# Kernel tuning notes

Hardware: AMD Instinct MI355X
Metric: run time of the kernel (lower is better)

The kernel has to match this reference:

```python
import jax, jax.numpy as jnp
import numpy as np

B, S, D, H, F = 64, 256, 512, 8, 2048
NB = 2
L = NB + 2 * NB  # blocks_1 (NB) + blocks_2 (2*NB) = 6 attention layers
DH = D // H
FC1, FC2 = 512, 256  # final_fc_dim, final_fc_dim // 2


def setup_inputs() -> dict:
    key = jax.random.key(0)
    ks = jax.random.split(key, 32)
    w = lambda k, shape, s: jax.random.normal(k, shape, dtype=jnp.float32) * s
    sD = D ** -0.5
    return {
        "q_embed_data": w(ks[0], (B, S, D), 1.0),
        "qa_embed_data": w(ks[1], (B, S, D), 1.0),
        "Wq": w(ks[2], (L, D, D), sD), "bq": jnp.zeros((L, D), jnp.float32),
        "Wk": w(ks[3], (L, D, D), sD), "bk": jnp.zeros((L, D), jnp.float32),
        "Wv": w(ks[4], (L, D, D), sD), "bv": jnp.zeros((L, D), jnp.float32),
        "Wo": w(ks[5], (L, D, D), sD), "bo": jnp.zeros((L, D), jnp.float32),
        "gammas": w(ks[6], (L, H), 1.0),
        "ln1_g": jnp.ones((L, D), jnp.float32), "ln1_b": jnp.zeros((L, D), jnp.float32),
        "W1": w(ks[7], (L, D, F), sD), "b1": jnp.zeros((L, F), jnp.float32),
        "W2": w(ks[8], (L, F, D), F ** -0.5), "b2": jnp.zeros((L, D), jnp.float32),
        "ln2_g": jnp.ones((L, D), jnp.float32), "ln2_b": jnp.zeros((L, D), jnp.float32),
        "O1": w(ks[9], (2 * D, FC1), (2 * D) ** -0.5), "bO1": jnp.zeros((FC1,), jnp.float32),
        "O2": w(ks[10], (FC1, FC2), FC1 ** -0.5), "bO2": jnp.zeros((FC2,), jnp.float32),
        "O3": w(ks[11], (FC2, 1), FC2 ** -0.5), "bO3": jnp.zeros((1,), jnp.float32),
    }


def _layer_norm(x, g, b):
    mu = x.mean(-1, keepdims=True)
    var = ((x - mu) ** 2).mean(-1, keepdims=True)
    return (x - mu) * jax.lax.rsqrt(var + 1e-5) * g + b


def _akt_attention(q, k, v, mask, gamma, zero_pad):
    # q,k,v: [B,H,S,DH]; mask: [S,S] bool; gamma: [H]
    neg = jnp.float32(-1e32)
    scores = jnp.einsum('bhqd,bhkd->bhqk', q, k) / np.sqrt(DH).astype(np.float32)
    # monotonic distance-decay (detached in the original): softmax'd scores -> cumulative distance
    sm = jax.nn.softmax(jnp.where(mask, scores, neg), axis=-1) * mask
    sm = jax.lax.stop_gradient(sm)
    distcum = jnp.cumsum(sm, axis=-1)
    disttot = jnp.sum(sm, axis=-1, keepdims=True)
    idx = jnp.arange(S)
    pos = jnp.abs(idx[:, None] - idx[None, :]).astype(jnp.float32)  # |x1 - x2|
    dist = jnp.sqrt(jnp.clip((disttot - distcum) * pos, 0.0, None))
    g = -jax.nn.softplus(gamma)[None, :, None, None]
    total_effect = jnp.clip(jnp.exp(dist * g), 1e-5, 1e5)
    scores = jnp.where(mask, scores * total_effect, neg)
    attn = jax.nn.softmax(scores, axis=-1)
    if zero_pad:
        attn = attn.at[:, :, 0, :].set(0.0)  # zero first query row
    out = jnp.einsum('bhqk,bhkd->bhqd', attn, v)
    return out, attn


def reference(q_embed_data, qa_embed_data, Wq, bq, Wk, bk, Wv, bv, Wo, bo, gammas,
              ln1_g, ln1_b, W1, b1, W2, b2, ln2_g, ln2_b, O1, bO1, O2, bO2, O3, bO3):
    idx = jnp.arange(S)
    mask_incl = idx[:, None] >= idx[None, :]  # mask==1: current + past
    mask_excl = idx[:, None] > idx[None, :]   # mask==0: strictly past

    def block(i, query, key_, vals, incl, zero_pad, apply_pos):
        proj = lambda x, W, b: (x @ W + b).reshape(B, S, H, DH).transpose(0, 2, 1, 3)
        qh, kh, vh = proj(query, Wq[i], bq[i]), proj(key_, Wk[i], bk[i]), proj(vals, Wv[i], bv[i])
        o, attn = _akt_attention(qh, kh, vh, mask_incl if incl else mask_excl, gammas[i], zero_pad)
        o = o.transpose(0, 2, 1, 3).reshape(B, S, D) @ Wo[i] + bo[i]
        q2 = _layer_norm(query + o, ln1_g[i], ln1_b[i])
        if apply_pos:
            h = jax.nn.relu(q2 @ W1[i] + b1[i]) @ W2[i] + b2[i]
            q2 = _layer_norm(q2 + h, ln2_g[i], ln2_b[i])
        return q2, attn

    y = qa_embed_data
    x = q_embed_data
    li = 0
    for _ in range(NB):  # blocks_1: knowledge encoder, self-attn, mask=1
        y, _ = block(li, y, y, y, incl=True, zero_pad=False, apply_pos=True)
        li += 1
    attn = None
    flag_first = True
    for _ in range(2 * NB):  # blocks_2: alternating question self-attn / knowledge retriever
        if flag_first:
            x, _ = block(li, x, x, x, incl=True, zero_pad=False, apply_pos=False)
            flag_first = False
        else:
            x, attn = block(li, x, x, y, incl=False, zero_pad=True, apply_pos=True)
            flag_first = True
        li += 1

    concat_q = jnp.concatenate([x, q_embed_data], axis=-1)  # [B,S,2D]
    h = jax.nn.relu(concat_q @ O1 + bO1)
    h = jax.nn.relu(h @ O2 + bO2)
    preds = jax.nn.sigmoid((h @ O3 + bO3)[..., 0])  # [B,S]
    return preds
```

## Files before the change

kernel.cpp:

```cpp
#include <hip/hip_runtime.h>

typedef unsigned short u16;
typedef unsigned int u32;
typedef short short8 __attribute__((ext_vector_type(8)));
typedef float f32x4 __attribute__((ext_vector_type(4)));

#define DEV static __device__ __forceinline__

DEV u16 f2bf(float f) {
  u32 u = __builtin_bit_cast(u32, f);
  u32 r = u + 0x7FFFu + ((u >> 16) & 1u);
  return (u16)(r >> 16);
}
DEV float bf2f(u16 h) { u32 u = ((u32)h) << 16; return __builtin_bit_cast(float, u); }

DEV u32 cvtpk(float lo, float hi_) {
  u32 r;
  asm("v_cvt_pk_bf16_f32 %0, %1, %2" : "=v"(r) : "v"(lo), "v"(hi_));
  return r;
}

DEV void async16(const u16* g, u16* l) {
  __builtin_amdgcn_global_load_lds((const __attribute__((address_space(1))) void*)g,
                                   (__attribute__((address_space(3))) void*)l, 16, 0, 0);
}

template<bool RELU, bool OUTBF, bool RESID, bool SPLIT3>
__global__ __launch_bounds__(256, 2) void gemm_kernel(
    const u16* __restrict__ A, const u16* __restrict__ A2, int KA,
    int lda, int lda2,
    const u16* __restrict__ Bt, int K,
    const float* __restrict__ bias, const float* __restrict__ resid,
    float* __restrict__ Cf, u16* __restrict__ Cb, u16* __restrict__ Cb2, u16* __restrict__ Cb3,
    int ldc)
{
  __shared__ u16 smem[2][16384];
  const int tid = threadIdx.x, wave = tid >> 6, lane = tid & 63;
  const int m0 = blockIdx.x * 128, n0 = blockIdx.y * 128;
  const int wr = wave >> 1, wc = wave & 1;
  const int lj = lane & 15, hi = lane >> 4;

  f32x4 acc[4][4];
  const f32x4 zz = {0.f, 0.f, 0.f, 0.f};
#pragma unroll
  for (int i = 0; i < 4; i++)
#pragma unroll
    for (int j = 0; j < 4; j++) acc[i][j] = zz;

  const int nkt = K / 64;

  auto stage = [&](int buf, int kt) {
    int kofs = kt * 64;
    const u16* sa; int la;
    if (kofs < KA) { sa = A + kofs; la = lda; }
    else           { sa = A2 + (kofs - KA); la = lda2; }
#pragma unroll
    for (int i = 0; i < 8; i++) {
      int c = wave * 8 + i;
      if (c < 16) {
        const u16* g = sa + (size_t)(m0 + c * 8 + (lane >> 3)) * la + (lane & 7) * 8;
        async16(g, &smem[buf][c * 512]);
      } else {
        const u16* g = Bt + (size_t)(n0 + (c - 16) * 8 + (lane >> 3)) * K + kofs + (lane & 7) * 8;
        async16(g, &smem[buf][c * 512]);
      }
    }
  };

  stage(0, 0);
  int cur = 0;
  for (int kt = 0; kt < nkt; kt++) {
    __syncthreads();
    if (kt + 1 < nkt) stage(cur ^ 1, kt + 1);
    const u16* la_ = &smem[cur][0];
    const u16* lb_ = &smem[cur][8192];
#pragma unroll
    for (int ks = 0; ks < 2; ks++) {
      short8 af[4], bfr[4];
#pragma unroll
      for (int mi = 0; mi < 4; mi++)
        af[mi] = *(const short8*)(la_ + (wr * 64 + mi * 16 + lj) * 64 + ks * 32 + hi * 8);
#pragma unroll
      for (int ni = 0; ni < 4; ni++)
        bfr[ni] = *(const short8*)(lb_ + (wc * 64 + ni * 16 + lj) * 64 + ks * 32 + hi * 8);
#pragma unroll
      for (int mi = 0; mi < 4; mi++)
#pragma unroll
        for (int ni = 0; ni < 4; ni++)
          acc[mi][ni] = __builtin_amdgcn_mfma_f32_16x16x32_bf16(af[mi], bfr[ni], acc[mi][ni], 0, 0, 0);
    }
    cur ^= 1;
  }

  u16* outB = Cb;
  int nloc = n0;
  if (SPLIT3) {
    int sec = n0 >> 9;
    outB = (sec == 0) ? Cb : (sec == 1) ? Cb2 : Cb3;
    nloc = n0 & 511;
  }

  float bv[4];
#pragma unroll
  for (int ni = 0; ni < 4; ni++) bv[ni] = bias[n0 + wc * 64 + ni * 16 + lj];
#pragma unroll
  for (int mi = 0; mi < 4; mi++)
#pragma unroll
    for (int r = 0; r < 4; r++) {
      int row = m0 + wr * 64 + mi * 16 + hi * 4 + r;
      size_t rb = (size_t)row * ldc;
#pragma unroll
      for (int ni = 0; ni < 4; ni++) {
        int col = nloc + wc * 64 + ni * 16 + lj;
        float v = acc[mi][ni][r] + bv[ni];
        if (RESID) v += resid[rb + col];
        if (RELU) v = fmaxf(v, 0.f);
        if (OUTBF) outB[rb + col] = f2bf(v);
        else Cf[rb + col] = v;
      }
    }
}

template<bool INCL, bool ZP>
__global__ __launch_bounds__(512) void attn_kernel(
    const u16* __restrict__ qb, const u16* __restrict__ kb, const u16* __restrict__ vb,
    u16* __restrict__ ob, const float* __restrict__ gammas, int li)
{
  __shared__ u16 smem[32768];
  const int tid = threadIdx.x, wave = tid >> 6, lane = tid & 63;
  const int h = blockIdx.x, b = blockIdx.y;
  const int lj = lane & 15, hi = lane >> 4;
  const size_t rowbase = (size_t)b * 256 * 512 + h * 64;

#pragma unroll
  for (int p = 0; p < 2; p++) {
    int r2 = p * 128 + (tid >> 3) * 2;
    int cc = (tid & 7) * 8;
    union { uint4 v; u16 e[8]; } v0, v1;
    uint4 k0 = *(const uint4*)(kb + rowbase + (size_t)r2 * 512 + cc);
    uint4 k1 = *(const uint4*)(kb + rowbase + (size_t)(r2 + 1) * 512 + cc);
    v0.v = *(const uint4*)(vb + rowbase + (size_t)r2 * 512 + cc);
    v1.v = *(const uint4*)(vb + rowbase + (size_t)(r2 + 1) * 512 + cc);
    *(uint4*)((char*)smem + r2 * 128 + ((cc * 2) ^ ((r2 & 7) << 4))) = k0;
    *(uint4*)((char*)smem + (r2 + 1) * 128 + ((cc * 2) ^ (((r2 + 1) & 7) << 4))) = k1;
#pragma unroll
    for (int i = 0; i < 8; i++) {
      int d = cc + i;
      u32 pk = (u32)v0.e[i] | ((u32)v1.e[i] << 16);
      *(u32*)((char*)smem + 32768 + d * 512 + ((2 * r2) ^ ((d & 7) << 4))) = pk;
    }
  }

  const int qt0 = wave, qt1 = 15 - wave;

  short8 qfa[2][2];
#pragma unroll
  for (int cf = 0; cf < 2; cf++) {
    int t = cf ? qt1 : qt0;
#pragma unroll
    for (int s = 0; s < 2; s++)
      qfa[cf][s] = *(const short8*)(qb + rowbase + (size_t)(t * 16 + lj) * 512 + s * 32 + hi * 8);
  }

  float gm = gammas[li * 8 + h];
  float geff = -(gm > 20.f ? gm : log1pf(__expf(gm)));

  __syncthreads();

  const f32x4 zz = {0.f, 0.f, 0.f, 0.f};
  const int hsel = hi >> 1;
  const int sbase = lj + 32 * (hi & 1);

#pragma unroll
  for (int cf = 0; cf < 2; cf++) {
    const int t = cf ? qt1 : qt0;
    const int qb0 = t * 16;
    const int q = qb0 + lj;
    const int nrf = t + 1;
    const int nsp = (t + 2) >> 1;

    f32x4 acc[16], E[16];
#pragma unroll
    for (int rf = 0; rf < 16; rf++) acc[rf] = zz;

#pragma unroll
    for (int rf = 0; rf < 16; rf++) {
      if (rf >= nrf) continue;
      int row = rf * 16 + lj;
#pragma unroll
      for (int s = 0; s < 2; s++) {
        short8 kf = *(const short8*)((char*)smem + row * 128 + ((s * 64 + hi * 16) ^ ((row & 7) << 4)));
        acc[rf] = __builtin_amdgcn_mfma_f32_16x16x32_bf16(kf, qfa[cf][s], acc[rf], 0, 0, 0);
      }
    }

    float mx = -1e30f;
#pragma unroll
    for (int rf = 0; rf < 16; rf++) {
      if (rf >= nrf) continue;
#pragma unroll
      for (int r = 0; r < 4; r++) {
        acc[rf][r] *= 0.125f;
        int k = rf * 16 + hi * 4 + r;
        bool valid = INCL ? (k <= q) : (k < q);
        mx = fmaxf(mx, valid ? acc[rf][r] : -1e30f);
      }
    }
    mx = fmaxf(mx, __shfl_xor(mx, 16));
    mx = fmaxf(mx, __shfl_xor(mx, 32));
    float sum = 0.f;
#pragma unroll
    for (int rf = 0; rf < 16; rf++) {
      if (rf >= nrf) continue;
#pragma unroll
      for (int r = 0; r < 4; r++) {
        int k = rf * 16 + hi * 4 + r;
        bool valid = INCL ? (k <= q) : (k < q);
        float ev = valid ? __expf(acc[rf][r] - mx) : 0.f;
        E[rf][r] = ev;
        sum += ev;
      }
    }
    sum += __shfl_xor(sum, 16);
    sum += __shfl_xor(sum, 32);
    float inv1 = sum > 0.f ? 1.f / sum : 0.f;
    float dtot = sum > 0.f ? 1.f : 0.f;

    float run = 0.f;
#pragma unroll
    for (int rf = 0; rf < 16; rf++) {
      if (rf >= nrf) continue;
      float p[4];
      float pa = 0.f;
#pragma unroll
      for (int r = 0; r < 4; r++) {
        pa += E[rf][r] * inv1;
        p[r] = pa;
      }
      float tl = p[3];
      float v = tl;
      float u1 = __shfl_up(v, 16); v += (hi >= 1) ? u1 : 0.f;
      float u2 = __shfl_up(v, 32); v += (hi >= 2) ? u2 : 0.f;
      float T = __shfl(v, lj + 48);
      float cbase = run + (v - tl);
#pragma unroll
      for (int r = 0; r < 4; r++) {
        int k = rf * 16 + hi * 4 + r;
        bool valid = INCL ? (k <= q) : (k < q);
        float tail = fmaxf(dtot - (cbase + p[r]), 0.f);
        float pos = (float)(q - k);
        float dist = sqrtf(tail * pos);
        float te = fmaxf(__expf(dist * geff), 1e-5f);
        acc[rf][r] = valid ? acc[rf][r] * te : -1e32f;
      }
      run += T;
    }

    float mx2 = -3.0e38f;
#pragma unroll
    for (int rf = 0; rf < 16; rf++) {
      if (rf >= nrf) continue;
#pragma unroll
      for (int r = 0; r < 4; r++) mx2 = fmaxf(mx2, acc[rf][r]);
    }
    mx2 = fmaxf(mx2, __shfl_xor(mx2, 16));
    mx2 = fmaxf(mx2, __shfl_xor(mx2, 32));
    float sum2 = 0.f;
#pragma unroll
    for (int rf = 0; rf < 16; rf++) {
      if (rf >= nrf) continue;
#pragma unroll
      for (int r = 0; r < 4; r++) {
        float ev = __expf(acc[rf][r] - mx2);
        acc[rf][r] = ev;
        sum2 += ev;
      }
    }
    sum2 += __shfl_xor(sum2, 16);
    sum2 += __shfl_xor(sum2, 32);
    float inv = 1.f / sum2;
    if (ZP) { if (q == 0) inv = 0.f; }
#pragma unroll
    for (int rf = 0; rf < 16; rf++) {
      if (rf >= nrf) continue;
#pragma unroll
      for (int r = 0; r < 4; r++) acc[rf][r] *= inv;
    }

    f32x4 oacc[4];
#pragma unroll
    for (int j = 0; j < 4; j++) oacc[j] = zz;

#pragma unroll
    for (int sp = 0; sp < 8; sp++) {
      if (sp >= nsp) continue;
      u32 a0 = cvtpk(acc[2 * sp][0],     acc[2 * sp][1]);
      u32 a1 = cvtpk(acc[2 * sp][2],     acc[2 * sp][3]);
      u32 b0 = cvtpk(acc[2 * sp + 1][0], acc[2 * sp + 1][1]);
      u32 b1 = cvtpk(acc[2 * sp + 1][2], acc[2 * sp + 1][3]);
      u32 pw[4];
#pragma unroll
      for (int tt = 0; tt < 4; tt++) {
        int src = sbase + 16 * (tt >> 1);
        u32 za = (u32)__shfl((int)((tt & 1) ? a1 : a0), src);
        u32 zb = (u32)__shfl((int)((tt & 1) ? b1 : b0), src);
        pw[tt] = hsel ? zb : za;
      }
      short8 pf = __builtin_bit_cast(short8, *(uint4*)pw);
#pragma unroll
      for (int nf = 0; nf < 4; nf++) {
        int d = nf * 16 + lj;
        short8 vf = *(const short8*)((char*)smem + 32768 + d * 512 + ((sp * 64 + hi * 16) ^ ((d & 7) << 4)));
        oacc[nf] = __builtin_amdgcn_mfma_f32_16x16x32_bf16(pf, vf, oacc[nf], 0, 0, 0);
      }
    }

#pragma unroll
    for (int r = 0; r < 4; r++) {
      int qr = qb0 + hi * 4 + r;
      size_t obase = (size_t)(b * 256 + qr) * 512 + h * 64;
#pragma unroll
      for (int nf = 0; nf < 4; nf++)
        ob[obase + nf * 16 + lj] = f2bf(oacc[nf][r]);
    }
  }
}

__global__ __launch_bounds__(256) void ln_kernel(const float* __restrict__ x,
    const float* __restrict__ g, const float* __restrict__ bt,
    float* __restrict__ outF, u16* __restrict__ outB)
{
  int row = blockIdx.x * 4 + (threadIdx.x >> 6), lane = threadIdx.x & 63;
  const float* xr = x + (size_t)row * 512 + lane * 8;
  float4 a = *(const float4*)xr;
  float4 c = *(const float4*)(xr + 4);
  float s = a.x + a.y + a.z + a.w + c.x + c.y + c.z + c.w;
  float q = a.x*a.x + a.y*a.y + a.z*a.z + a.w*a.w + c.x*c.x + c.y*c.y + c.z*c.z + c.w*c.w;
#pragma unroll
  for (int m = 1; m <= 32; m <<= 1) { s += __shfl_xor(s, m); q += __shfl_xor(q, m); }
  float mu = s * (1.f / 512.f);
  float var = q * (1.f / 512.f) - mu * mu;
  float rs = rsqrtf(fmaxf(var, 0.f) + 1e-5f);
  const float* gr = g + lane * 8; const float* br = bt + lane * 8;
  float4 g0 = *(const float4*)gr, g1v = *(const float4*)(gr + 4);
  float4 b0 = *(const float4*)br, b1v = *(const float4*)(br + 4);
  float y[8];
  y[0]=(a.x-mu)*rs*g0.x+b0.x; y[1]=(a.y-mu)*rs*g0.y+b0.y; y[2]=(a.z-mu)*rs*g0.z+b0.z; y[3]=(a.w-mu)*rs*g0.w+b0.w;
  y[4]=(c.x-mu)*rs*g1v.x+b1v.x; y[5]=(c.y-mu)*rs*g1v.y+b1v.y; y[6]=(c.z-mu)*rs*g1v.z+b1v.z; y[7]=(c.w-mu)*rs*g1v.w+b1v.w;
  float* of = outF + (size_t)row * 512 + lane * 8;
  *(float4*)of = make_float4(y[0], y[1], y[2], y[3]);
  *(float4*)(of + 4) = make_float4(y[4], y[5], y[6], y[7]);
  union { uint4 v; u16 e[8]; } pk;
#pragma unroll
  for (int i = 0; i < 8; i++) pk.e[i] = f2bf(y[i]);
  *(uint4*)(outB + (size_t)row * 512 + lane * 8) = pk.v;
}

__global__ void cvt_kernel(const float* __restrict__ in, u16* __restrict__ out, int n8)
{
  int i = blockIdx.x * 256 + threadIdx.x;
  if (i >= n8) return;
  float4 a = ((const float4*)in)[2 * i], c = ((const float4*)in)[2 * i + 1];
  union { uint4 v; u16 e[8]; } pk;
  pk.e[0]=f2bf(a.x); pk.e[1]=f2bf(a.y); pk.e[2]=f2bf(a.z); pk.e[3]=f2bf(a.w);
  pk.e[4]=f2bf(c.x); pk.e[5]=f2bf(c.y); pk.e[6]=f2bf(c.z); pk.e[7]=f2bf(c.w);
  ((uint4*)out)[i] = pk.v;
}

__global__ void trans_kernel(const float* __restrict__ in, u16* __restrict__ out,
                             int R, int C, size_t istr, size_t ostr)
{
  __shared__ float tile[32][33];
  in += (size_t)blockIdx.z * istr;
  out += (size_t)blockIdx.z * ostr;
  int c0 = blockIdx.x * 32, r0 = blockIdx.y * 32;
  int tx = threadIdx.x & 31, ty = threadIdx.x >> 5;
#pragma unroll
  for (int i = 0; i < 4; i++) tile[ty + i * 8][tx] = in[(size_t)(r0 + ty + i * 8) * C + c0 + tx];
  __syncthreads();
#pragma unroll
  for (int i = 0; i < 4; i++) out[(size_t)(c0 + ty + i * 8) * R + r0 + tx] = f2bf(tile[tx][ty + i * 8]);
}

__global__ void bias_concat_kernel(const float* __restrict__ bq, const float* __restrict__ bk,
                                   const float* __restrict__ bv, float* __restrict__ out)
{
  int t = blockIdx.x * 256 + threadIdx.x;
  if (t >= 6 * 1536) return;
  int li = t / 1536, c = t % 1536;
  float v = (c < 512) ? bq[li * 512 + c]
          : (c < 1024) ? bk[li * 512 + c - 512]
                       : bv[li * 512 + c - 1024];
  out[t] = v;
}

__global__ __launch_bounds__(256) void pred_kernel(const u16* __restrict__ h2,
    const float* __restrict__ O3, const float* __restrict__ bO3, float* __restrict__ out)
{
  int row = blockIdx.x * 4 + (threadIdx.x >> 6), lane = threadIdx.x & 63;
  union { uint2 v; u16 e[4]; } hv;
  hv.v = *(const uint2*)(h2 + (size_t)row * 256 + lane * 4);
  float d = 0.f;
#pragma unroll
  for (int i = 0; i < 4; i++) d += bf2f(hv.e[i]) * O3[lane * 4 + i];
#pragma unroll
  for (int m = 1; m <= 32; m <<= 1) d += __shfl_xor(d, m);
  if (lane == 0) out[row] = 1.f / (1.f + expf(-(d + bO3[0])));
}

extern "C" void kernel_launch(void* const* d_in, const int* in_sizes, int n_in,
                              void* d_out, int out_size, void* d_ws, size_t ws_size,
                              hipStream_t stream)
{
  const float* qe   = (const float*)d_in[0];
  const float* qa   = (const float*)d_in[1];
  const float* Wq   = (const float*)d_in[2];  const float* bq  = (const float*)d_in[3];
  const float* Wk   = (const float*)d_in[4];  const float* bk  = (const float*)d_in[5];
  const float* Wv   = (const float*)d_in[6];  const float* bv  = (const float*)d_in[7];
  const float* Wo   = (const float*)d_in[8];  const float* bo  = (const float*)d_in[9];
  const float* gam  = (const float*)d_in[10];
  const float* ln1g = (const float*)d_in[11]; const float* ln1b = (const float*)d_in[12];
  const float* W1   = (const float*)d_in[13]; const float* b1  = (const float*)d_in[14];
  const float* W2   = (const float*)d_in[15]; const float* b2  = (const float*)d_in[16];
  const float* ln2g = (const float*)d_in[17]; const float* ln2b = (const float*)d_in[18];
  const float* O1   = (const float*)d_in[19]; const float* bO1 = (const float*)d_in[20];
  const float* O2   = (const float*)d_in[21]; const float* bO2 = (const float*)d_in[22];
  const float* O3   = (const float*)d_in[23]; const float* bO3 = (const float*)d_in[24];
  float* preds = (float*)d_out;

  const int M = 16384;
  const int BIG = 0x3fffffff;
  char* ws = (char*)d_ws;
  size_t off = 0;
  auto alloc = [&](size_t bytes) { char* p = ws + off; off += (bytes + 255) & ~(size_t)255; return p; };

  u16* wqkvt = (u16*)alloc((size_t)6*1536*512*2);
  u16* wot   = (u16*)alloc((size_t)6*512*512*2);
  u16* w1t   = (u16*)alloc((size_t)6*2048*512*2);
  u16* w2t   = (u16*)alloc((size_t)6*512*2048*2);
  u16* o1t   = (u16*)alloc((size_t)512*1024*2);
  u16* o2t   = (u16*)alloc((size_t)256*512*2);
  float* bqkv = (float*)alloc((size_t)6*1536*4);
  u16* qx  = (u16*)alloc((size_t)M*512*2);
  u16* sA  = (u16*)alloc((size_t)M*512*2);
  u16* sB  = (u16*)alloc((size_t)M*512*2);
  float* g1 = (float*)alloc((size_t)M*512*4);
  u16* region = (u16*)alloc((size_t)M*2048*2);
  u16* qbf = region;
  u16* kbf = region + (size_t)M*512;
  u16* vbf = region + (size_t)2*M*512;
  u16* obf = region + (size_t)3*M*512;
  u16* h1  = region;
  u16* hd1 = region;
  u16* hd2 = region + (size_t)2*M*512;
  (void)ws_size; (void)in_sizes; (void)n_in; (void)out_size;

  trans_kernel<<<dim3(16, 16, 6), 256, 0, stream>>>(Wq, wqkvt,                          512, 512,  (size_t)512*512,  (size_t)1536*512);
  trans_kernel<<<dim3(16, 16, 6), 256, 0, stream>>>(Wk, wqkvt + (size_t)512*512,        512, 512,  (size_t)512*512,  (size_t)1536*512);
  trans_kernel<<<dim3(16, 16, 6), 256, 0, stream>>>(Wv, wqkvt + (size_t)1024*512,       512, 512,  (size_t)512*512,  (size_t)1536*512);
  trans_kernel<<<dim3(16, 16, 6), 256, 0, stream>>>(Wo, wot,                            512, 512,  (size_t)512*512,  (size_t)512*512);
  trans_kernel<<<dim3(64, 16, 6), 256, 0, stream>>>(W1, w1t,                            512, 2048, (size_t)512*2048, (size_t)2048*512);
  trans_kernel<<<dim3(16, 64, 6), 256, 0, stream>>>(W2, w2t,                            2048, 512, (size_t)2048*512, (size_t)512*2048);
  trans_kernel<<<dim3(16, 32, 1), 256, 0, stream>>>(O1, o1t,                            1024, 512, 0, 0);
  trans_kernel<<<dim3(8, 16, 1),  256, 0, stream>>>(O2, o2t,                            512, 256,  0, 0);
  bias_concat_kernel<<<36, 256, 0, stream>>>(bq, bk, bv, bqkv);
  cvt_kernel<<<4096, 256, 0, stream>>>(qe, qx, M * 512 / 8);
  cvt_kernel<<<4096, 256, 0, stream>>>(qa, sA, M * 512 / 8);

  const u16* curB = sA;
  const float* curF = qa;
  const u16* yfin = nullptr;
  const dim3 gP(128, 4), gF1(128, 16), gA(8, 64);

  for (int li = 0; li < 6; li++) {
    bool ffn  = (li == 0 || li == 1 || li == 3 || li == 5);
    bool excl = (li == 3 || li == 5);
    size_t wqkv_off = (size_t)li * 1536 * 512;

    if (!excl) {
      gemm_kernel<false, true, false, true><<<dim3(128, 12), 256, 0, stream>>>(
          curB, curB, BIG, 512, 512, wqkvt + wqkv_off, 512, bqkv + li * 1536,
          nullptr, nullptr, qbf, kbf, vbf, 512);
    } else {
      gemm_kernel<false, true, false, true><<<dim3(128, 8), 256, 0, stream>>>(
          curB, curB, BIG, 512, 512, wqkvt + wqkv_off, 512, bqkv + li * 1536,
          nullptr, nullptr, qbf, kbf, nullptr, 512);
      gemm_kernel<false, true, false, false><<<dim3(128, 4), 256, 0, stream>>>(
          yfin, yfin, BIG, 512, 512, wqkvt + wqkv_off + (size_t)1024 * 512, 512, bv + li * 512,
          nullptr, nullptr, vbf, nullptr, nullptr, 512);
    }

    if (!excl) attn_kernel<true,  false><<<gA, 512, 0, stream>>>(qbf, kbf, vbf, obf, gam, li);
    else       attn_kernel<false, true ><<<gA, 512, 0, stream>>>(qbf, kbf, vbf, obf, gam, li);

    gemm_kernel<false, false, true, false><<<gP, 256, 0, stream>>>(
        obf, obf, BIG, 512, 512, wot + (size_t)li * 512 * 512, 512, bo + li * 512,
        curF, g1, nullptr, nullptr, nullptr, 512);

    ln_kernel<<<4096, 256, 0, stream>>>(g1, ln1g + li * 512, ln1b + li * 512, g1, sB);
    curB = sB; curF = g1;

    if (ffn) {
      gemm_kernel<true, true, false, false><<<gF1, 256, 0, stream>>>(
          curB, curB, BIG, 512, 512, w1t + (size_t)li * 2048 * 512, 512, b1 + li * 2048,
          nullptr, nullptr, h1, nullptr, nullptr, 2048);
      gemm_kernel<false, false, true, false><<<gP, 256, 0, stream>>>(
          h1, h1, BIG, 2048, 2048, w2t + (size_t)li * 512 * 2048, 2048, b2 + li * 512,
          g1, g1, nullptr, nullptr, nullptr, 512);
      u16* nB = (li < 2) ? sA : sB;
      ln_kernel<<<4096, 256, 0, stream>>>(g1, ln2g + li * 512, ln2b + li * 512, g1, nB);
      curB = nB;
    }
    if (li == 1) { yfin = curB; curB = qx; curF = qe; }
  }

  gemm_kernel<true, true, false, false><<<dim3(128, 4), 256, 0, stream>>>(
      curB, qx, 512, 512, 512, o1t, 1024, bO1, nullptr, nullptr, hd1, nullptr, nullptr, 512);
  gemm_kernel<true, true, false, false><<<dim3(128, 2), 256, 0, stream>>>(
      hd1, hd1, BIG, 512, 512, o2t, 512, bO2, nullptr, nullptr, hd2, nullptr, nullptr, 256);
  pred_kernel<<<4096, 256, 0, stream>>>(hd2, O3, bO3, preds);
}
```

Before: 1.385 ms.

## Add 256x256-tile 512-thread GEMM for QKV and FFN1 projections

Introduces a new bf16 MFMA GEMM kernel with 256x256 output tiles, 8 waves, double-buffered async global-to-LDS loads with XOR swizzle, and per-phase prefetch interleaved with compute. It replaces the 128-tile GEMM for the fused QKV projection and the first FFN layer, aiming for more data reuse per loaded tile and fewer blocks. In exchange it uses 128KB of LDS and a large accumulator array per thread, which limits occupancy, and it launches only a few hundred blocks.

```diff
diff --git a/kernel.cpp b/kernel.cpp
--- a/kernel.cpp
+++ b/kernel.cpp
@@ -117,6 +117,120 @@
         if (RELU) v = fmaxf(v, 0.f);
         if (OUTBF) outB[rb + col] = f2bf(v);
         else Cf[rb + col] = v;
+      }
+    }
+}
+
+template<bool RELU, bool SPLIT3>
+__global__ __launch_bounds__(512) void gemm256_kernel(
+    const u16* __restrict__ A, int lda,
+    const u16* __restrict__ Bt, int K,
+    const float* __restrict__ bias,
+    u16* __restrict__ Cb, u16* __restrict__ Cb2, u16* __restrict__ Cb3, int ldc)
+{
+  __shared__ u16 smem[65536];
+  const int tid = threadIdx.x, wave = tid >> 6, lane = tid & 63;
+  const int m0 = blockIdx.x * 256, n0 = blockIdx.y * 256;
+  const int wm = wave >> 2, wn = wave & 3;
+  const int lj = lane & 15, hi = lane >> 4;
+  const int srow = wave * 8 + (lane >> 3);
+  const int schunk = (lane & 7) ^ ((lane >> 3) & 7);
+
+  f32x4 acc[8][4];
+  const f32x4 zz = {0.f, 0.f, 0.f, 0.f};
+#pragma unroll
+  for (int i = 0; i < 8; i++)
+#pragma unroll
+    for (int j = 0; j < 4; j++) acc[i][j] = zz;
+
+  const int nkt = K / 64;
+
+  auto stageA = [&](int buf, int kt, int seg) {
+    const u16* g = A + (size_t)(m0 + seg * 64 + srow) * lda + kt * 64 + schunk * 8;
+    async16(g, &smem[buf * 16384 + (seg * 64 + wave * 8) * 64]);
+  };
+  auto stageB = [&](int buf, int kt, int seg) {
+    const u16* g = Bt + (size_t)(n0 + seg * 64 + srow) * K + kt * 64 + schunk * 8;
+    async16(g, &smem[32768 + buf * 16384 + (seg * 64 + wave * 8) * 64]);
+  };
+
+#pragma unroll
+  for (int seg = 0; seg < 4; seg++) stageA(0, 0, seg);
+#pragma unroll
+  for (int seg = 0; seg < 4; seg++) stageB(0, 0, seg);
+
+  int cur = 0;
+  for (int t = 0; t < nkt; t++) {
+    const bool pf = (t + 1 < nkt);
+    const char* aB = (const char*)smem + cur * 32768;
+    const char* bB = (const char*)smem + 65536 + cur * 32768;
+#pragma unroll
+    for (int ph = 0; ph < 4; ph++) {
+      const int mh = ph >> 1, nh = ph & 1;
+      if (pf) {
+        if (ph < 2) { stageA(cur ^ 1, t + 1, ph * 2); stageA(cur ^ 1, t + 1, ph * 2 + 1); }
+        else        { stageB(cur ^ 1, t + 1, (ph - 2) * 2); stageB(cur ^ 1, t + 1, (ph - 2) * 2 + 1); }
+      }
+      if (ph == 0) {
+        if (pf) asm volatile("s_waitcnt vmcnt(2)" ::: "memory");
+        else    asm volatile("s_waitcnt vmcnt(0)" ::: "memory");
+      }
+      __builtin_amdgcn_s_barrier();
+
+      short8 af[4][2], bfr[2][2];
+#pragma unroll
+      for (int mi = 0; mi < 4; mi++) {
+        int row = wm * 128 + (mh * 4 + mi) * 16 + lj;
+#pragma unroll
+        for (int ks = 0; ks < 2; ks++)
+          af[mi][ks] = *(const short8*)(aB + row * 128 + ((ks * 64 + hi * 16) ^ ((row & 7) << 4)));
+      }
+#pragma unroll
+      for (int ni = 0; ni < 2; ni++) {
+        int row = wn * 64 + (nh * 2 + ni) * 16 + lj;
+#pragma unroll
+        for (int ks = 0; ks < 2; ks++)
+          bfr[ni][ks] = *(const short8*)(bB + row * 128 + ((ks * 64 + hi * 16) ^ ((row & 7) << 4)));
+      }
+      __builtin_amdgcn_s_setprio(1);
+#pragma unroll
+      for (int mi = 0; mi < 4; mi++)
+#pragma unroll
+        for (int ni = 0; ni < 2; ni++)
+#pragma unroll
+          for (int ks = 0; ks < 2; ks++)
+            acc[mh * 4 + mi][nh * 2 + ni] =
+                __builtin_amdgcn_mfma_f32_16x16x32_bf16(af[mi][ks], bfr[ni][ks],
+                                                        acc[mh * 4 + mi][nh * 2 + ni], 0, 0, 0);
+      __builtin_amdgcn_s_setprio(0);
+      __builtin_amdgcn_s_barrier();
+    }
+    cur ^= 1;
+  }
+
+  u16* outB = Cb;
+  int nloc = n0;
+  if (SPLIT3) {
+    int sec = n0 >> 9;
+    outB = (sec == 0) ? Cb : (sec == 1) ? Cb2 : Cb3;
+    nloc = n0 & 511;
+  }
+
+  float bv[4];
+#pragma unroll
+  for (int ni = 0; ni < 4; ni++) bv[ni] = bias[n0 + wn * 64 + ni * 16 + lj];
+#pragma unroll
+  for (int mi = 0; mi < 8; mi++)
+#pragma unroll
+    for (int r = 0; r < 4; r++) {
+      int row = m0 + wm * 128 + mi * 16 + hi * 4 + r;
+      size_t rb = (size_t)row * ldc;
+#pragma unroll
+      for (int ni = 0; ni < 4; ni++) {
+        int col = nloc + wn * 64 + ni * 16 + lj;
+        float v = acc[mi][ni][r] + bv[ni];
+        if (RELU) v = fmaxf(v, 0.f);
+        outB[rb + col] = f2bf(v);
       }
     }
 }
@@ -470,7 +584,7 @@
   const u16* curB = sA;
   const float* curF = qa;
   const u16* yfin = nullptr;
-  const dim3 gP(128, 4), gF1(128, 16), gA(8, 64);
+  const dim3 gP(128, 4), gA(8, 64);
 
   for (int li = 0; li < 6; li++) {
     bool ffn  = (li == 0 || li == 1 || li == 3 || li == 5);
@@ -478,13 +592,11 @@
     size_t wqkv_off = (size_t)li * 1536 * 512;
 
     if (!excl) {
-      gemm_kernel<false, true, false, true><<<dim3(128, 12), 256, 0, stream>>>(
-          curB, curB, BIG, 512, 512, wqkvt + wqkv_off, 512, bqkv + li * 1536,
-          nullptr, nullptr, qbf, kbf, vbf, 512);
+      gemm256_kernel<false, true><<<dim3(64, 6), 512, 0, stream>>>(
+          curB, 512, wqkvt + wqkv_off, 512, bqkv + li * 1536, qbf, kbf, vbf, 512);
     } else {
-      gemm_kernel<false, true, false, true><<<dim3(128, 8), 256, 0, stream>>>(
-          curB, curB, BIG, 512, 512, wqkvt + wqkv_off, 512, bqkv + li * 1536,
-          nullptr, nullptr, qbf, kbf, nullptr, 512);
+      gemm256_kernel<false, true><<<dim3(64, 4), 512, 0, stream>>>(
+          curB, 512, wqkvt + wqkv_off, 512, bqkv + li * 1536, qbf, kbf, nullptr, 512);
       gemm_kernel<false, true, false, false><<<dim3(128, 4), 256, 0, stream>>>(
           yfin, yfin, BIG, 512, 512, wqkvt + wqkv_off + (size_t)1024 * 512, 512, bv + li * 512,
           nullptr, nullptr, vbf, nullptr, nullptr, 512);
@@ -501,9 +613,8 @@
     curB = sB; curF = g1;
 
     if (ffn) {
-      gemm_kernel<true, true, false, false><<<gF1, 256, 0, stream>>>(
-          curB, curB, BIG, 512, 512, w1t + (size_t)li * 2048 * 512, 512, b1 + li * 2048,
-          nullptr, nullptr, h1, nullptr, nullptr, 2048);
+      gemm256_kernel<true, false><<<dim3(64, 8), 512, 0, stream>>>(
+          curB, 512, w1t + (size_t)li * 2048 * 512, 512, b1 + li * 2048, h1, nullptr, nullptr, 2048);
       gemm_kernel<false, false, true, false><<<gP, 256, 0, stream>>>(
           h1, h1, BIG, 2048, 2048, w2t + (size_t)li * 512 * 2048, 2048, b2 + li * 512,
           g1, g1, nullptr, nullptr, nullptr, 512);
```

After: 1.331 ms. 1.04x faster.
